# Kernel tuning notes

Measured on AMD Instinct MI355X. Metric: run time of the kernel, lower is better.

Reference implementation:

```python
import jax, jax.numpy as jnp
import numpy as np

N, C, T, V, K = 32, 256, 64, 25, 3   # batch, in_channels, frames, joints, adjacency partitions
D = 256                               # out_channels
KT = 9                                # temporal kernel size
PAD = (KT - 1) // 2
EPS = 1e-5                            # BatchNorm eps (torch default)


def setup_inputs() -> dict:
    key = jax.random.key(0)
    ks = jax.random.split(key, 5)
    x = jax.random.normal(ks[0], (N, C, T, V), jnp.float32)
    A = jax.random.uniform(ks[1], (K, V, V), jnp.float32)           # learnable adjacency
    W_gcn = jax.random.normal(ks[2], (K, D, C), jnp.float32) * (2.0 / C) ** 0.5  # K stacked 1x1 convs
    b_gcn = jnp.zeros((K, D), jnp.float32)
    W_tcn = jax.random.normal(ks[3], (D, D, KT, 1), jnp.float32) * (2.0 / (D * KT)) ** 0.5  # kaiming fan_out
    b_tcn = jnp.zeros((D,), jnp.float32)
    gamma = jnp.ones((D,), jnp.float32)   # bn_init(bn, 1)
    beta = jnp.zeros((D,), jnp.float32)
    return dict(x=x, A=A, W_gcn=W_gcn, b_gcn=b_gcn, W_tcn=W_tcn,
                b_tcn=b_tcn, gamma=gamma, beta=beta)


def reference(x, A, W_gcn, b_gcn, W_tcn, b_tcn, gamma, beta):
    # ---- GCN: per-partition 1x1 conv over channels, then graph aggregation via A[k], summed over k ----
    # y[k,n,d,t,v] = sum_c W_gcn[k,d,c] * x[n,c,t,v] + b_gcn[k,d]
    y = jnp.einsum('kdc,nctv->kndtv', W_gcn, x) + b_gcn[:, None, :, None, None]
    # aggregate neighbors: sum_v y[k,n,d,t,v] * A[k,v,w], accumulated over partitions k
    y = jnp.einsum('kndtv,kvw->ndtw', y, A)        # [N, D, T, V]

    # ---- TCN: (9,1) temporal conv + BatchNorm2d (batch statistics) ----
    z = jax.lax.conv_general_dilated(
        y, W_tcn, window_strides=(1, 1), padding=((PAD, PAD), (0, 0)),
        dimension_numbers=('NCHW', 'OIHW', 'NCHW'))
    z = z + b_tcn[None, :, None, None]
    mean = jnp.mean(z, axis=(0, 2, 3), keepdims=True)
    var = jnp.mean((z - mean) ** 2, axis=(0, 2, 3), keepdims=True)  # biased, as torch BN training fwd
    z = gamma[None, :, None, None] * (z - mean) * jax.lax.rsqrt(var + EPS) + beta[None, :, None, None]

    # ---- residual (identity branch: in==out, stride==1) + ReLU ----
    return jax.nn.relu(z + x)
```

## Files before the change

kernel.cpp:

```cpp
#include <hip/hip_runtime.h>
#include <math.h>

typedef unsigned short u16;
typedef short v8s __attribute__((ext_vector_type(8)));
typedef float v4f __attribute__((ext_vector_type(4)));

#define AS1 __attribute__((address_space(1)))
#define AS3 __attribute__((address_space(3)))

__device__ __forceinline__ float bf2f(u16 u) {
    union { unsigned int i; float f; } c; c.i = ((unsigned int)u) << 16; return c.f;
}
__device__ __forceinline__ u16 f2bf(float f) {
    union { float f; unsigned int i; } c; c.f = f;
    unsigned int u = c.i;
    return (u16)((u + 0x7FFFu + ((u >> 16) & 1u)) >> 16);
}
__device__ __forceinline__ void gload_lds16(const void* g, void* l) {
    __builtin_amdgcn_global_load_lds((const AS1 void*)(uintptr_t)g,
                                     (AS3 void*)(unsigned int)(uintptr_t)l,
                                     16, 0, 0);
}

#define Nn 32
#define Tt 64
#define Vv 25
#define NP 51200
#define NBLK 400

__global__ __launch_bounds__(256) void prep_kernel(
    const float* __restrict__ Wg, const float* __restrict__ Wt,
    const float* __restrict__ A, const float* __restrict__ bg,
    u16* __restrict__ Wgb, u16* __restrict__ Wtb,
    float* __restrict__ bias2, float* __restrict__ zpad)
{
    const int idx = blockIdx.x * 256 + threadIdx.x;
    const int stride = gridDim.x * 256;
    for (int i = idx; i < 256 * 2304; i += stride) {
        int d = i / 2304, r = i - d * 2304, dt = r >> 8, c = r & 255;
        Wtb[i] = f2bf(Wt[(d * 256 + c) * 9 + dt]);
    }
    for (int i = idx; i < 256 * 768; i += stride) {
        int d = i / 768, r = i - d * 768, k = r >> 8, c = r & 255;
        Wgb[i] = f2bf(Wg[(k * 256 + d) * 256 + c]);
    }
    for (int i = idx; i < 25 * 256; i += stride) {
        int w = i >> 8, d = i & 255;
        float s = 0.f;
        for (int k = 0; k < 3; ++k) {
            float cs = 0.f;
            for (int v = 0; v < 25; ++v) cs += A[(k * 25 + v) * 25 + w];
            s += bg[k * 256 + d] * cs;
        }
        bias2[i] = s;
    }
    for (int i = idx; i < 256; i += stride) zpad[i] = 0.f;
}

__global__ __launch_bounds__(256) void xa_kernel(
    const float* __restrict__ x, const float* __restrict__ A,
    u16* __restrict__ xa2)
{
    const int t = blockIdx.x, n = blockIdx.y;
    const int tid = threadIdx.x;
    __shared__ float xs[256 * 25];

    for (int i = tid; i < 6400; i += 256) {
        int c = i / 25, v = i - c * 25;
        xs[i] = x[((n * 256 + c) * 64 + t) * 25 + v];
    }
    __syncthreads();

    float xr[25];
    #pragma unroll
    for (int v = 0; v < 25; ++v) xr[v] = xs[tid * 25 + v];

    const size_t pbase = ((size_t)n * 64 + t) * 25;
    #pragma unroll 1
    for (int k = 0; k < 3; ++k) {
        float o[25];
        #pragma unroll
        for (int w = 0; w < 25; ++w) {
            float acc = 0.f;
            #pragma unroll
            for (int v = 0; v < 25; ++v)
                acc = fmaf(xr[v], A[(k * 25 + v) * 25 + w], acc);
            o[w] = acc;
        }
        u16* dst = xa2 + k * 256 + tid;
        #pragma unroll
        for (int w = 0; w < 25; ++w)
            dst[(pbase + w) * 768] = f2bf(o[w]);
    }
}

template<int KTOT, bool TCN>
__global__ __launch_bounds__(512, 2) void gemm_kernel(
    const u16* __restrict__ Ad, const u16* __restrict__ Bw,
    const float* __restrict__ bias, u16* __restrict__ outB,
    float* __restrict__ psum, float* __restrict__ psq,
    const u16* __restrict__ zpad)
{
    __shared__ u16 smem[24576];
    u16* As = smem;
    u16* Bs = smem + 8192;

    const int tid = threadIdx.x;
    const int wid = tid >> 6, lane = tid & 63;
    const int lr = lane & 15, hk = lane >> 4;
    const int wm = wid >> 2, wn = wid & 3;
    const int blk = blockIdx.x;
    const int rA = lane >> 3, sA = lane & 7;

    v4f acc[4][4];
    const v4f vzero = {0.f, 0.f, 0.f, 0.f};
    #pragma unroll
    for (int mf = 0; mf < 4; ++mf)
        #pragma unroll
        for (int nf = 0; nf < 4; ++nf) acc[mf][nf] = vzero;

    for (int kt = 0; kt < KTOT / 64; ++kt) {
        #pragma unroll
        for (int i = 0; i < 2; ++i) {
            const int ch = wid + i * 8;
            const int row = ch * 8 + rA;
            const int p = blk * 128 + row;
            const int ss = sA ^ (row & 7);
            const u16* src;
            if (TCN) {
                const int dt = kt >> 2, c0 = (kt & 3) << 6;
                const int tv = p % 1600, t = tv / 25;
                const int tp = t + dt - 4;
                const int p2 = p + (dt - 4) * 25;
                src = ((unsigned)tp < 64u) ? (Ad + (size_t)p2 * 256 + c0 + ss * 8) : zpad;
            } else {
                src = Ad + (size_t)p * 768 + kt * 64 + ss * 8;
            }
            gload_lds16(src, (char*)As + ch * 1024);
        }
        #pragma unroll
        for (int i = 0; i < 4; ++i) {
            const int ch = wid + i * 8;
            const int d = ch * 8 + rA;
            const int ss = sA ^ (d & 7);
            gload_lds16(Bw + (size_t)d * KTOT + kt * 64 + ss * 8, (char*)Bs + ch * 1024);
        }
        __syncthreads();

        v8s a[4][2], b[4][2];
        #pragma unroll
        for (int mf = 0; mf < 4; ++mf)
            #pragma unroll
            for (int kk = 0; kk < 2; ++kk) {
                const int row = wm * 64 + mf * 16 + lr;
                const int slot = kk * 4 + hk;
                a[mf][kk] = *(const v8s*)((const char*)As + row * 128 + ((slot ^ (row & 7)) << 4));
            }
        #pragma unroll
        for (int nf = 0; nf < 4; ++nf)
            #pragma unroll
            for (int kk = 0; kk < 2; ++kk) {
                const int row = wn * 64 + nf * 16 + lr;
                const int slot = kk * 4 + hk;
                b[nf][kk] = *(const v8s*)((const char*)Bs + row * 128 + ((slot ^ (row & 7)) << 4));
            }
        #pragma unroll
        for (int kk = 0; kk < 2; ++kk)
            #pragma unroll
            for (int mf = 0; mf < 4; ++mf)
                #pragma unroll
                for (int nf = 0; nf < 4; ++nf)
                    acc[mf][nf] = __builtin_amdgcn_mfma_f32_16x16x32_bf16(
                        a[mf][kk], b[nf][kk], acc[mf][nf], 0, 0, 0);
        __syncthreads();
    }

    if (!TCN) {
        #pragma unroll
        for (int mf = 0; mf < 4; ++mf) {
            #pragma unroll
            for (int j = 0; j < 4; ++j) {
                const int p = blk * 128 + wm * 64 + mf * 16 + hk * 4 + j;
                const int w = p % 25;
                #pragma unroll
                for (int nf = 0; nf < 4; ++nf) {
                    const int d = wn * 64 + nf * 16 + lr;
                    outB[(size_t)p * 256 + d] = f2bf(acc[mf][nf][j] + bias[w * 256 + d]);
                }
            }
        }
    } else {
        float s[4], q[4];
        #pragma unroll
        for (int nf = 0; nf < 4; ++nf) {
            const int d = wn * 64 + nf * 16 + lr;
            const float bb = bias[d];
            s[nf] = 0.f; q[nf] = 0.f;
            #pragma unroll
            for (int mf = 0; mf < 4; ++mf) {
                #pragma unroll
                for (int j = 0; j < 4; ++j) {
                    const int p = blk * 128 + wm * 64 + mf * 16 + hk * 4 + j;
                    const float zz = acc[mf][nf][j] + bb;
                    outB[(size_t)p * 256 + d] = f2bf(zz);
                    s[nf] += zz; q[nf] += zz * zz;
                }
            }
            s[nf] += __shfl_xor(s[nf], 16); s[nf] += __shfl_xor(s[nf], 32);
            q[nf] += __shfl_xor(q[nf], 16); q[nf] += __shfl_xor(q[nf], 32);
        }
        __syncthreads();
        float* red = (float*)smem;
        if (hk == 0) {
            #pragma unroll
            for (int nf = 0; nf < 4; ++nf) {
                const int d = wn * 64 + nf * 16 + lr;
                red[wm * 256 + d] = s[nf];
                red[512 + wm * 256 + d] = q[nf];
            }
        }
        __syncthreads();
        if (tid < 256) {
            psum[(size_t)tid * NBLK + blk] = red[tid] + red[256 + tid];
            psq[(size_t)tid * NBLK + blk]  = red[512 + tid] + red[768 + tid];
        }
    }
}

__global__ __launch_bounds__(256) void bn_stats_kernel(
    const float* __restrict__ psum, const float* __restrict__ psq,
    const float* __restrict__ gamma, const float* __restrict__ beta,
    float* __restrict__ scale, float* __restrict__ shift)
{
    const int d = blockIdx.x, tid = threadIdx.x;
    float s = 0.f, q = 0.f;
    for (int i = tid; i < NBLK; i += 256) {
        s += psum[(size_t)d * NBLK + i];
        q += psq[(size_t)d * NBLK + i];
    }
    #pragma unroll
    for (int off = 32; off; off >>= 1) {
        s += __shfl_down(s, off);
        q += __shfl_down(q, off);
    }
    __shared__ float rs[4], rq[4];
    if ((tid & 63) == 0) { rs[tid >> 6] = s; rq[tid >> 6] = q; }
    __syncthreads();
    if (tid == 0) {
        s = rs[0] + rs[1] + rs[2] + rs[3];
        q = rq[0] + rq[1] + rq[2] + rq[3];
        const float mean = s / 51200.f;
        const float var = q / 51200.f - mean * mean;
        const float inv = rsqrtf(var + 1e-5f);
        scale[d] = gamma[d] * inv;
        shift[d] = beta[d] - gamma[d] * inv * mean;
    }
}

__global__ __launch_bounds__(256) void bn_apply_kernel(
    const u16* __restrict__ zb, const float* __restrict__ x,
    const float* __restrict__ scale, const float* __restrict__ shift,
    float* __restrict__ out)
{
    const int chunk = blockIdx.x;
    const int n = blockIdx.y;
    const int tid = threadIdx.x;
    __shared__ u16 zs[128 * 66];
    const size_t p0 = (size_t)n * 1600 + chunk * 64;

    for (int half = 0; half < 2; ++half) {
        const int d0 = half * 128;
        if (half) __syncthreads();
        for (int i = tid; i < 128 * 64; i += 256) {
            const int pl = i >> 7, dl = i & 127;
            zs[dl * 66 + pl] = zb[(p0 + pl) * 256 + d0 + dl];
        }
        __syncthreads();
        for (int i = tid; i < 128 * 64; i += 256) {
            const int dl = i >> 6, j = i & 63;
            const int d = d0 + dl;
            const size_t addr = ((size_t)n * 256 + d) * 1600 + chunk * 64 + j;
            const float r = bf2f(zs[dl * 66 + j]) * scale[d] + shift[d] + x[addr];
            out[addr] = fmaxf(r, 0.f);
        }
    }
}

extern "C" void kernel_launch(void* const* d_in, const int* in_sizes, int n_in,
                              void* d_out, int out_size, void* d_ws, size_t ws_size,
                              hipStream_t stream)
{
    const float* x     = (const float*)d_in[0];
    const float* A     = (const float*)d_in[1];
    const float* Wg    = (const float*)d_in[2];
    const float* bg    = (const float*)d_in[3];
    const float* Wt    = (const float*)d_in[4];
    const float* bt    = (const float*)d_in[5];
    const float* gamma = (const float*)d_in[6];
    const float* beta  = (const float*)d_in[7];
    float* out = (float*)d_out;

    char* w = (char*)d_ws;
    u16*   xa2   = (u16*)(w);
    u16*   y2T   = (u16*)(w + 78643200);
    u16*   zb    = (u16*)(w + 104857600);
    u16*   Wgb   = (u16*)(w + 131072000);
    u16*   Wtb   = (u16*)(w + 131465216);
    float* bias2 = (float*)(w + 132644864);
    float* psum  = (float*)(w + 132670464);
    float* psq   = (float*)(w + 133080064);
    float* scale = (float*)(w + 133489664);
    float* shift = (float*)(w + 133490688);
    float* zpad  = (float*)(w + 133491712);

    prep_kernel<<<512, 256, 0, stream>>>(Wg, Wt, A, bg, Wgb, Wtb, bias2, zpad);
    xa_kernel<<<dim3(64, 32), 256, 0, stream>>>(x, A, xa2);
    gemm_kernel<768, false><<<NBLK, 512, 0, stream>>>(xa2, Wgb, bias2, y2T,
                                                      nullptr, nullptr, (const u16*)zpad);
    gemm_kernel<2304, true><<<NBLK, 512, 0, stream>>>(y2T, Wtb, bt, zb,
                                                      psum, psq, (const u16*)zpad);
    bn_stats_kernel<<<256, 256, 0, stream>>>(psum, psq, gamma, beta, scale, shift);
    bn_apply_kernel<<<dim3(25, 32), 256, 0, stream>>>(zb, x, scale, shift, out);
}
```

Measured before the change: 169.8 us.

## Enlarge GEMM tiles to 256x256 with XCD-aware block remapping

Both GEMM kernels now use 256-row by 256-column output tiles per block instead of 128x256, so each warp computes 8x4 MFMA fragments and the grid halves to 200 blocks. Block indices are remapped so consecutive M tiles land on the same XCD, and the prep kernel launches fewer blocks. This raises arithmetic intensity per LDS load and cuts redundant weight traffic, at the cost of more accumulator registers (occupancy hint dropped) and 200 blocks on 256 CUs leaving some CUs idle.

```diff
diff --git a/kernel.cpp b/kernel.cpp
--- a/kernel.cpp
+++ b/kernel.cpp
@@ -26,7 +26,7 @@
 #define Tt 64
 #define Vv 25
 #define NP 51200
-#define NBLK 400
+#define NBLK 200
 
 __global__ __launch_bounds__(256) void prep_kernel(
     const float* __restrict__ Wg, const float* __restrict__ Wt,
@@ -95,92 +95,89 @@
 }
 
 template<int KTOT, bool TCN>
-__global__ __launch_bounds__(512, 2) void gemm_kernel(
+__global__ __launch_bounds__(512) void gemm_kernel(
     const u16* __restrict__ Ad, const u16* __restrict__ Bw,
     const float* __restrict__ bias, u16* __restrict__ outB,
     float* __restrict__ psum, float* __restrict__ psq,
     const u16* __restrict__ zpad)
 {
-    __shared__ u16 smem[24576];
-    u16* As = smem;
-    u16* Bs = smem + 8192;
+    constexpr int NT = KTOT / 64;
+    __shared__ u16 smem[32768];
 
     const int tid = threadIdx.x;
     const int wid = tid >> 6, lane = tid & 63;
     const int lr = lane & 15, hk = lane >> 4;
     const int wm = wid >> 2, wn = wid & 3;
-    const int blk = blockIdx.x;
     const int rA = lane >> 3, sA = lane & 7;
 
-    v4f acc[4][4];
+    const int orig = blockIdx.x;
+    const int m = (orig & 7) * 25 + (orig >> 3);
+
+    u16* As = smem;
+    u16* Bs = smem + 16384;
+
+    v4f acc[8][4];
     const v4f vzero = {0.f, 0.f, 0.f, 0.f};
     #pragma unroll
-    for (int mf = 0; mf < 4; ++mf)
+    for (int mf = 0; mf < 8; ++mf)
         #pragma unroll
         for (int nf = 0; nf < 4; ++nf) acc[mf][nf] = vzero;
 
-    for (int kt = 0; kt < KTOT / 64; ++kt) {
-        #pragma unroll
-        for (int i = 0; i < 2; ++i) {
+    for (int kt = 0; kt < NT; ++kt) {
+        #pragma unroll
+        for (int i = 0; i < 4; ++i) {
             const int ch = wid + i * 8;
             const int row = ch * 8 + rA;
-            const int p = blk * 128 + row;
-            const int ss = sA ^ (row & 7);
-            const u16* src;
+            const int ss = sA ^ rA;
+            const u16* srcA;
             if (TCN) {
                 const int dt = kt >> 2, c0 = (kt & 3) << 6;
-                const int tv = p % 1600, t = tv / 25;
+                const int p = m * 256 + row;
+                const int t = (p % 1600) / 25;
                 const int tp = t + dt - 4;
-                const int p2 = p + (dt - 4) * 25;
-                src = ((unsigned)tp < 64u) ? (Ad + (size_t)p2 * 256 + c0 + ss * 8) : zpad;
+                srcA = ((unsigned)tp < 64u)
+                     ? (Ad + (size_t)(p + (dt - 4) * 25) * 256 + c0 + ss * 8)
+                     : zpad;
             } else {
-                src = Ad + (size_t)p * 768 + kt * 64 + ss * 8;
-            }
-            gload_lds16(src, (char*)As + ch * 1024);
-        }
-        #pragma unroll
-        for (int i = 0; i < 4; ++i) {
-            const int ch = wid + i * 8;
-            const int d = ch * 8 + rA;
-            const int ss = sA ^ (d & 7);
-            gload_lds16(Bw + (size_t)d * KTOT + kt * 64 + ss * 8, (char*)Bs + ch * 1024);
-        }
-        __syncthreads();
-
-        v8s a[4][2], b[4][2];
-        #pragma unroll
-        for (int mf = 0; mf < 4; ++mf)
-            #pragma unroll
-            for (int kk = 0; kk < 2; ++kk) {
-                const int row = wm * 64 + mf * 16 + lr;
+                srcA = Ad + (size_t)(m * 256 + row) * 768 + kt * 64 + ss * 8;
+            }
+            gload_lds16(srcA, (char*)As + ch * 1024);
+            gload_lds16(Bw + (size_t)row * KTOT + kt * 64 + ss * 8,
+                        (char*)Bs + ch * 1024);
+        }
+        __syncthreads();
+
+        #pragma unroll
+        for (int kk = 0; kk < 2; ++kk) {
+            v8s a[8], b[4];
+            #pragma unroll
+            for (int mf = 0; mf < 8; ++mf) {
+                const int row = wm * 128 + mf * 16 + lr;
                 const int slot = kk * 4 + hk;
-                a[mf][kk] = *(const v8s*)((const char*)As + row * 128 + ((slot ^ (row & 7)) << 4));
-            }
-        #pragma unroll
-        for (int nf = 0; nf < 4; ++nf)
-            #pragma unroll
-            for (int kk = 0; kk < 2; ++kk) {
+                a[mf] = *(const v8s*)((const char*)As + row * 128 + ((slot ^ (row & 7)) << 4));
+            }
+            #pragma unroll
+            for (int nf = 0; nf < 4; ++nf) {
                 const int row = wn * 64 + nf * 16 + lr;
                 const int slot = kk * 4 + hk;
-                b[nf][kk] = *(const v8s*)((const char*)Bs + row * 128 + ((slot ^ (row & 7)) << 4));
-            }
-        #pragma unroll
-        for (int kk = 0; kk < 2; ++kk)
-            #pragma unroll
-            for (int mf = 0; mf < 4; ++mf)
+                b[nf] = *(const v8s*)((const char*)Bs + row * 128 + ((slot ^ (row & 7)) << 4));
+            }
+            #pragma unroll
+            for (int mf = 0; mf < 8; ++mf)
                 #pragma unroll
                 for (int nf = 0; nf < 4; ++nf)
                     acc[mf][nf] = __builtin_amdgcn_mfma_f32_16x16x32_bf16(
-                        a[mf][kk], b[nf][kk], acc[mf][nf], 0, 0, 0);
+                        a[mf], b[nf], acc[mf][nf], 0, 0, 0);
+        }
         __syncthreads();
     }
 
     if (!TCN) {
         #pragma unroll
-        for (int mf = 0; mf < 4; ++mf) {
+        for (int mf = 0; mf < 8; ++mf) {
             #pragma unroll
             for (int j = 0; j < 4; ++j) {
-                const int p = blk * 128 + wm * 64 + mf * 16 + hk * 4 + j;
+                const int p = m * 256 + wm * 128 + mf * 16 + hk * 4 + j;
                 const int w = p % 25;
                 #pragma unroll
                 for (int nf = 0; nf < 4; ++nf) {
@@ -197,10 +194,10 @@
             const float bb = bias[d];
             s[nf] = 0.f; q[nf] = 0.f;
             #pragma unroll
-            for (int mf = 0; mf < 4; ++mf) {
+            for (int mf = 0; mf < 8; ++mf) {
                 #pragma unroll
                 for (int j = 0; j < 4; ++j) {
-                    const int p = blk * 128 + wm * 64 + mf * 16 + hk * 4 + j;
+                    const int p = m * 256 + wm * 128 + mf * 16 + hk * 4 + j;
                     const float zz = acc[mf][nf][j] + bb;
                     outB[(size_t)p * 256 + d] = f2bf(zz);
                     s[nf] += zz; q[nf] += zz * zz;
@@ -221,8 +218,8 @@
         }
         __syncthreads();
         if (tid < 256) {
-            psum[(size_t)tid * NBLK + blk] = red[tid] + red[256 + tid];
-            psq[(size_t)tid * NBLK + blk]  = red[512 + tid] + red[768 + tid];
+            psum[(size_t)tid * NBLK + m] = red[tid] + red[256 + tid];
+            psq[(size_t)tid * NBLK + m]  = red[512 + tid] + red[768 + tid];
         }
     }
 }
@@ -313,7 +310,7 @@
     float* shift = (float*)(w + 133490688);
     float* zpad  = (float*)(w + 133491712);
 
-    prep_kernel<<<512, 256, 0, stream>>>(Wg, Wt, A, bg, Wgb, Wtb, bias2, zpad);
+    prep_kernel<<<128, 256, 0, stream>>>(Wg, Wt, A, bg, Wgb, Wtb, bias2, zpad);
     xa_kernel<<<dim3(64, 32), 256, 0, stream>>>(x, A, xa2);
     gemm_kernel<768, false><<<NBLK, 512, 0, stream>>>(xa2, Wgb, bias2, y2T,
                                                       nullptr, nullptr, (const u16*)zpad);
```

Measured after the change: 196.8 us. +15.9%, slower.

## Restructure temporal conv GEMM to reuse a haloed LDS tile across taps

Applied to the files above, without the earlier changes.

The temporal convolution kernel now loads one 128-row activation tile plus a 104-row halo on each side into LDS once per 64-channel chunk. All 9 temporal taps are computed from that single tile by shifting the row index, instead of reloading an im2col slice for every tap. Weights are pre-permuted into MFMA fragment order and read straight from global memory into registers with double buffering, so B no longer goes through LDS. Boundary blocks zero the out-of-range tap fragments, and both GEMMs use a block index remap. The cost is a larger LDS footprint per block, extra work to load the halo, and a masked code path for blocks near sequence edges.

```diff
diff --git a/kernel.cpp b/kernel.cpp
--- a/kernel.cpp
+++ b/kernel.cpp
@@ -31,18 +31,22 @@
 __global__ __launch_bounds__(256) void prep_kernel(
     const float* __restrict__ Wg, const float* __restrict__ Wt,
     const float* __restrict__ A, const float* __restrict__ bg,
-    u16* __restrict__ Wgb, u16* __restrict__ Wtb,
+    u16* __restrict__ Wgb, u16* __restrict__ Bpt,
     float* __restrict__ bias2, float* __restrict__ zpad)
 {
     const int idx = blockIdx.x * 256 + threadIdx.x;
     const int stride = gridDim.x * 256;
-    for (int i = idx; i < 256 * 2304; i += stride) {
-        int d = i / 2304, r = i - d * 2304, dt = r >> 8, c = r & 255;
-        Wtb[i] = f2bf(Wt[(d * 256 + c) * 9 + dt]);
+    for (int i = idx; i < 589824; i += stride) {
+        const int e = i & 7, lane = (i >> 3) & 63, sub = i >> 9;
+        const int kk = sub & 1, nf = (sub >> 1) & 3, wn = (sub >> 3) & 3;
+        const int cc = (sub >> 5) & 3, dt = sub >> 7;
+        const int d = wn * 64 + nf * 16 + (lane & 15);
+        const int c = cc * 64 + kk * 32 + (lane >> 4) * 8 + e;
+        Bpt[i] = f2bf(Wt[(d * 256 + c) * 9 + dt]);
     }
     for (int i = idx; i < 256 * 768; i += stride) {
-        int d = i / 768, r = i - d * 768, k = r >> 8, c = r & 255;
-        Wgb[i] = f2bf(Wg[(k * 256 + d) * 256 + c]);
+        int d = i / 768, r = i - d * 768, k3 = r >> 8, c = r & 255;
+        Wgb[i] = f2bf(Wg[(k3 * 256 + d) * 256 + c]);
     }
     for (int i = idx; i < 25 * 256; i += stride) {
         int w = i >> 8, d = i & 255;
@@ -94,12 +98,9 @@
     }
 }
 
-template<int KTOT, bool TCN>
-__global__ __launch_bounds__(512, 2) void gemm_kernel(
+__global__ __launch_bounds__(512) void gemm1_kernel(
     const u16* __restrict__ Ad, const u16* __restrict__ Bw,
-    const float* __restrict__ bias, u16* __restrict__ outB,
-    float* __restrict__ psum, float* __restrict__ psq,
-    const u16* __restrict__ zpad)
+    const float* __restrict__ bias, u16* __restrict__ outB)
 {
     __shared__ u16 smem[24576];
     u16* As = smem;
@@ -109,8 +110,10 @@
     const int wid = tid >> 6, lane = tid & 63;
     const int lr = lane & 15, hk = lane >> 4;
     const int wm = wid >> 2, wn = wid & 3;
-    const int blk = blockIdx.x;
     const int rA = lane >> 3, sA = lane & 7;
+
+    const int orig = blockIdx.x;
+    const int m = (orig & 7) * 50 + (orig >> 3);
 
     v4f acc[4][4];
     const v4f vzero = {0.f, 0.f, 0.f, 0.f};
@@ -119,31 +122,22 @@
         #pragma unroll
         for (int nf = 0; nf < 4; ++nf) acc[mf][nf] = vzero;
 
-    for (int kt = 0; kt < KTOT / 64; ++kt) {
+    for (int kt = 0; kt < 12; ++kt) {
         #pragma unroll
         for (int i = 0; i < 2; ++i) {
             const int ch = wid + i * 8;
             const int row = ch * 8 + rA;
-            const int p = blk * 128 + row;
-            const int ss = sA ^ (row & 7);
-            const u16* src;
-            if (TCN) {
-                const int dt = kt >> 2, c0 = (kt & 3) << 6;
-                const int tv = p % 1600, t = tv / 25;
-                const int tp = t + dt - 4;
-                const int p2 = p + (dt - 4) * 25;
-                src = ((unsigned)tp < 64u) ? (Ad + (size_t)p2 * 256 + c0 + ss * 8) : zpad;
-            } else {
-                src = Ad + (size_t)p * 768 + kt * 64 + ss * 8;
-            }
-            gload_lds16(src, (char*)As + ch * 1024);
+            const int ss = sA ^ rA;
+            gload_lds16(Ad + (size_t)(m * 128 + row) * 768 + kt * 64 + ss * 8,
+                        (char*)As + ch * 1024);
         }
         #pragma unroll
         for (int i = 0; i < 4; ++i) {
             const int ch = wid + i * 8;
             const int d = ch * 8 + rA;
-            const int ss = sA ^ (d & 7);
-            gload_lds16(Bw + (size_t)d * KTOT + kt * 64 + ss * 8, (char*)Bs + ch * 1024);
+            const int ss = sA ^ rA;
+            gload_lds16(Bw + (size_t)d * 768 + kt * 64 + ss * 8,
+                        (char*)Bs + ch * 1024);
         }
         __syncthreads();
 
@@ -175,55 +169,149 @@
         __syncthreads();
     }
 
-    if (!TCN) {
+    #pragma unroll
+    for (int mf = 0; mf < 4; ++mf) {
+        #pragma unroll
+        for (int j = 0; j < 4; ++j) {
+            const int p = m * 128 + wm * 64 + mf * 16 + hk * 4 + j;
+            const int w = p % 25;
+            #pragma unroll
+            for (int nf = 0; nf < 4; ++nf) {
+                const int d = wn * 64 + nf * 16 + lr;
+                outB[(size_t)p * 256 + d] = f2bf(acc[mf][nf][j] + bias[w * 256 + d]);
+            }
+        }
+    }
+}
+
+__global__ __launch_bounds__(512) void tcn_halo_kernel(
+    const u16* __restrict__ y2T, const u16* __restrict__ Bpt,
+    const float* __restrict__ bt, u16* __restrict__ zb,
+    float* __restrict__ psum, float* __restrict__ psq,
+    const u16* __restrict__ zp)
+{
+    __shared__ u16 smem[21504];
+
+    const int tid = threadIdx.x;
+    const int wid = tid >> 6, lane = tid & 63;
+    const int lr = lane & 15, hk = lane >> 4;
+    const int wm = wid >> 2, wn = wid & 3;
+    const int rA = lane >> 3, sA = lane & 7;
+
+    const int orig = blockIdx.x;
+    const int m = (orig & 7) * 50 + (orig >> 3);
+
+    u16* As = smem;
+
+    v4f acc[4][4];
+    const v4f vzero = {0.f, 0.f, 0.f, 0.f};
+    #pragma unroll
+    for (int mf = 0; mf < 4; ++mf)
+        #pragma unroll
+        for (int nf = 0; nf < 4; ++nf) acc[mf][nf] = vzero;
+
+    int tt[4];
+    #pragma unroll
+    for (int mf = 0; mf < 4; ++mf)
+        tt[mf] = ((m * 128 + wm * 64 + mf * 16 + lr) % 1600) / 25;
+
+    const int r0 = (m * 128) % 1600;
+    const bool safe = (r0 >= 104) && (r0 <= 1368);
+
+#define BLOAD(bank, dtv, ccv)                                                  \
+    {                                                                          \
+        const u16* bw = Bpt + ((((dtv)*4 + (ccv)) * 4 + wn) << 12) + lane * 8; \
+        _Pragma("unroll")                                                      \
+        for (int nf = 0; nf < 4; ++nf)                                         \
+            _Pragma("unroll")                                                  \
+            for (int kk = 0; kk < 2; ++kk)                                     \
+                bb[bank][nf][kk] = *(const v8s*)(bw + ((nf * 2 + kk) << 9));   \
+    }
+
+#define CC_BODY(MASKED)                                                        \
+    _Pragma("unroll 1")                                                        \
+    for (int cc = 0; cc < 4; ++cc) {                                           \
+        if (cc) __syncthreads();                                               \
+        for (int ch = wid; ch < 42; ch += 8) {                                 \
+            const int row = ch * 8 + rA;                                       \
+            const int srow = m * 128 - 104 + row;                              \
+            const int ss = sA ^ rA;                                            \
+            const u16* src = ((unsigned)srow < 51200u)                         \
+                ? (y2T + (size_t)srow * 256 + cc * 64 + ss * 8) : zp;          \
+            gload_lds16(src, (char*)As + ch * 1024);                           \
+        }                                                                      \
+        __syncthreads();                                                       \
+        v8s bb[2][4][2];                                                       \
+        BLOAD(0, 0, cc)                                                        \
+        _Pragma("unroll")                                                      \
+        for (int dt = 0; dt < 9; ++dt) {                                       \
+            if (dt < 8) BLOAD((dt + 1) & 1, dt + 1, cc)                        \
+            v8s a[4][2];                                                       \
+            _Pragma("unroll")                                                  \
+            for (int mf = 0; mf < 4; ++mf)                                     \
+                _Pragma("unroll")                                              \
+                for (int kk = 0; kk < 2; ++kk) {                               \
+                    const int lrow = 104 + wm * 64 + mf * 16 + lr + (dt - 4) * 25; \
+                    const int slot = kk * 4 + hk;                              \
+                    a[mf][kk] = *(const v8s*)((const char*)As + lrow * 128 +   \
+                                              ((slot ^ (lrow & 7)) << 4));     \
+                }                                                              \
+            if (MASKED) {                                                      \
+                _Pragma("unroll")                                              \
+                for (int mf = 0; mf < 4; ++mf) {                               \
+                    const bool ok = (unsigned)(tt[mf] + dt - 4) < 64u;         \
+                    a[mf][0] = ok ? a[mf][0] : (v8s)(short)0;                  \
+                    a[mf][1] = ok ? a[mf][1] : (v8s)(short)0;                  \
+                }                                                              \
+            }                                                                  \
+            _Pragma("unroll")                                                  \
+            for (int kk = 0; kk < 2; ++kk)                                     \
+                _Pragma("unroll")                                              \
+                for (int mf = 0; mf < 4; ++mf)                                 \
+                    _Pragma("unroll")                                          \
+                    for (int nf = 0; nf < 4; ++nf)                             \
+                        acc[mf][nf] = __builtin_amdgcn_mfma_f32_16x16x32_bf16( \
+                            a[mf][kk], bb[dt & 1][nf][kk], acc[mf][nf], 0, 0, 0); \
+        }                                                                      \
+    }
+
+    if (safe) { CC_BODY(false) } else { CC_BODY(true) }
+#undef CC_BODY
+#undef BLOAD
+
+    float s[4], q[4];
+    #pragma unroll
+    for (int nf = 0; nf < 4; ++nf) {
+        const int d = wn * 64 + nf * 16 + lr;
+        const float bbv = bt[d];
+        s[nf] = 0.f; q[nf] = 0.f;
         #pragma unroll
         for (int mf = 0; mf < 4; ++mf) {
             #pragma unroll
             for (int j = 0; j < 4; ++j) {
-                const int p = blk * 128 + wm * 64 + mf * 16 + hk * 4 + j;
-                const int w = p % 25;
-                #pragma unroll
-                for (int nf = 0; nf < 4; ++nf) {
-                    const int d = wn * 64 + nf * 16 + lr;
-                    outB[(size_t)p * 256 + d] = f2bf(acc[mf][nf][j] + bias[w * 256 + d]);
-                }
+                const int p = m * 128 + wm * 64 + mf * 16 + hk * 4 + j;
+                const float zz = acc[mf][nf][j] + bbv;
+                zb[(size_t)p * 256 + d] = f2bf(zz);
+                s[nf] += zz; q[nf] += zz * zz;
             }
         }
-    } else {
-        float s[4], q[4];
+        s[nf] += __shfl_xor(s[nf], 16); s[nf] += __shfl_xor(s[nf], 32);
+        q[nf] += __shfl_xor(q[nf], 16); q[nf] += __shfl_xor(q[nf], 32);
+    }
+    __syncthreads();
+    float* red = (float*)smem;
+    if (hk == 0) {
         #pragma unroll
         for (int nf = 0; nf < 4; ++nf) {
             const int d = wn * 64 + nf * 16 + lr;
-            const float bb = bias[d];
-            s[nf] = 0.f; q[nf] = 0.f;
-            #pragma unroll
-            for (int mf = 0; mf < 4; ++mf) {
-                #pragma unroll
-                for (int j = 0; j < 4; ++j) {
-                    const int p = blk * 128 + wm * 64 + mf * 16 + hk * 4 + j;
-                    const float zz = acc[mf][nf][j] + bb;
-                    outB[(size_t)p * 256 + d] = f2bf(zz);
-                    s[nf] += zz; q[nf] += zz * zz;
-                }
-            }
-            s[nf] += __shfl_xor(s[nf], 16); s[nf] += __shfl_xor(s[nf], 32);
-            q[nf] += __shfl_xor(q[nf], 16); q[nf] += __shfl_xor(q[nf], 32);
-        }
-        __syncthreads();
-        float* red = (float*)smem;
-        if (hk == 0) {
-            #pragma unroll
-            for (int nf = 0; nf < 4; ++nf) {
-                const int d = wn * 64 + nf * 16 + lr;
-                red[wm * 256 + d] = s[nf];
-                red[512 + wm * 256 + d] = q[nf];
-            }
-        }
-        __syncthreads();
-        if (tid < 256) {
-            psum[(size_t)tid * NBLK + blk] = red[tid] + red[256 + tid];
-            psq[(size_t)tid * NBLK + blk]  = red[512 + tid] + red[768 + tid];
-        }
+            red[wm * 256 + d] = s[nf];
+            red[512 + wm * 256 + d] = q[nf];
+        }
+    }
+    __syncthreads();
+    if (tid < 256) {
+        psum[(size_t)tid * NBLK + m] = red[tid] + red[256 + tid];
+        psq[(size_t)tid * NBLK + m]  = red[512 + tid] + red[768 + tid];
     }
 }
 
@@ -305,7 +393,7 @@
     u16*   y2T   = (u16*)(w + 78643200);
     u16*   zb    = (u16*)(w + 104857600);
     u16*   Wgb   = (u16*)(w + 131072000);
-    u16*   Wtb   = (u16*)(w + 131465216);
+    u16*   Bpt   = (u16*)(w + 131465216);
     float* bias2 = (float*)(w + 132644864);
     float* psum  = (float*)(w + 132670464);
     float* psq   = (float*)(w + 133080064);
@@ -313,12 +401,11 @@
     float* shift = (float*)(w + 133490688);
     float* zpad  = (float*)(w + 133491712);
 
-    prep_kernel<<<512, 256, 0, stream>>>(Wg, Wt, A, bg, Wgb, Wtb, bias2, zpad);
+    prep_kernel<<<256, 256, 0, stream>>>(Wg, Wt, A, bg, Wgb, Bpt, bias2, zpad);
     xa_kernel<<<dim3(64, 32), 256, 0, stream>>>(x, A, xa2);
-    gemm_kernel<768, false><<<NBLK, 512, 0, stream>>>(xa2, Wgb, bias2, y2T,
-                                                      nullptr, nullptr, (const u16*)zpad);
-    gemm_kernel<2304, true><<<NBLK, 512, 0, stream>>>(y2T, Wtb, bt, zb,
-                                                      psum, psq, (const u16*)zpad);
+    gemm1_kernel<<<NBLK, 512, 0, stream>>>(xa2, Wgb, bias2, y2T);
+    tcn_halo_kernel<<<NBLK, 512, 0, stream>>>(y2T, Bpt, bt, zb, psum, psq,
+                                              (const u16*)zpad);
     bn_stats_kernel<<<256, 256, 0, stream>>>(psum, psq, gamma, beta, scale, shift);
     bn_apply_kernel<<<dim3(25, 32), 256, 0, stream>>>(zb, x, scale, shift, out);
 }
```

New measurement: 172.7 us. No clear change (+1.7%).

## Split TCN GEMM K dimension in two and move BN stats to separate pass

Applied to the files above, without the earlier changes.

Splits the temporal-conv GEMM over its reduction dimension into two halves run as 800 blocks, each writing a bf16 partial result, so the 400-block grid fills more of the GPU. BN statistics move out of the GEMM epilogue into a new zsum kernel that adds the two partials, and bn_apply now sums both partials itself. It also adds an XCD-aware block index swizzle, drops the min-occupancy launch bound, and halves the prep grid. In exchange it adds extra memory traffic for the second partial buffer and an extra kernel launch, and it rounds each partial to bf16 before summing.

```diff
diff --git a/kernel.cpp b/kernel.cpp
--- a/kernel.cpp
+++ b/kernel.cpp
@@ -94,12 +94,9 @@
     }
 }
 
-template<int KTOT, bool TCN>
-__global__ __launch_bounds__(512, 2) void gemm_kernel(
+__global__ __launch_bounds__(512) void gemm1_kernel(
     const u16* __restrict__ Ad, const u16* __restrict__ Bw,
-    const float* __restrict__ bias, u16* __restrict__ outB,
-    float* __restrict__ psum, float* __restrict__ psq,
-    const u16* __restrict__ zpad)
+    const float* __restrict__ bias, u16* __restrict__ outB)
 {
     __shared__ u16 smem[24576];
     u16* As = smem;
@@ -109,8 +106,10 @@
     const int wid = tid >> 6, lane = tid & 63;
     const int lr = lane & 15, hk = lane >> 4;
     const int wm = wid >> 2, wn = wid & 3;
-    const int blk = blockIdx.x;
     const int rA = lane >> 3, sA = lane & 7;
+
+    const int orig = blockIdx.x;
+    const int m = (orig & 7) * 50 + (orig >> 3);
 
     v4f acc[4][4];
     const v4f vzero = {0.f, 0.f, 0.f, 0.f};
@@ -119,31 +118,22 @@
         #pragma unroll
         for (int nf = 0; nf < 4; ++nf) acc[mf][nf] = vzero;
 
-    for (int kt = 0; kt < KTOT / 64; ++kt) {
+    for (int kt = 0; kt < 12; ++kt) {
         #pragma unroll
         for (int i = 0; i < 2; ++i) {
             const int ch = wid + i * 8;
             const int row = ch * 8 + rA;
-            const int p = blk * 128 + row;
-            const int ss = sA ^ (row & 7);
-            const u16* src;
-            if (TCN) {
-                const int dt = kt >> 2, c0 = (kt & 3) << 6;
-                const int tv = p % 1600, t = tv / 25;
-                const int tp = t + dt - 4;
-                const int p2 = p + (dt - 4) * 25;
-                src = ((unsigned)tp < 64u) ? (Ad + (size_t)p2 * 256 + c0 + ss * 8) : zpad;
-            } else {
-                src = Ad + (size_t)p * 768 + kt * 64 + ss * 8;
-            }
-            gload_lds16(src, (char*)As + ch * 1024);
+            const int ss = sA ^ rA;
+            gload_lds16(Ad + (size_t)(m * 128 + row) * 768 + kt * 64 + ss * 8,
+                        (char*)As + ch * 1024);
         }
         #pragma unroll
         for (int i = 0; i < 4; ++i) {
             const int ch = wid + i * 8;
             const int d = ch * 8 + rA;
-            const int ss = sA ^ (d & 7);
-            gload_lds16(Bw + (size_t)d * KTOT + kt * 64 + ss * 8, (char*)Bs + ch * 1024);
+            const int ss = sA ^ rA;
+            gload_lds16(Bw + (size_t)d * 768 + kt * 64 + ss * 8,
+                        (char*)Bs + ch * 1024);
         }
         __syncthreads();
 
@@ -175,56 +165,133 @@
         __syncthreads();
     }
 
-    if (!TCN) {
-        #pragma unroll
-        for (int mf = 0; mf < 4; ++mf) {
-            #pragma unroll
-            for (int j = 0; j < 4; ++j) {
-                const int p = blk * 128 + wm * 64 + mf * 16 + hk * 4 + j;
-                const int w = p % 25;
-                #pragma unroll
-                for (int nf = 0; nf < 4; ++nf) {
-                    const int d = wn * 64 + nf * 16 + lr;
-                    outB[(size_t)p * 256 + d] = f2bf(acc[mf][nf][j] + bias[w * 256 + d]);
-                }
-            }
-        }
-    } else {
-        float s[4], q[4];
-        #pragma unroll
-        for (int nf = 0; nf < 4; ++nf) {
-            const int d = wn * 64 + nf * 16 + lr;
-            const float bb = bias[d];
-            s[nf] = 0.f; q[nf] = 0.f;
-            #pragma unroll
-            for (int mf = 0; mf < 4; ++mf) {
-                #pragma unroll
-                for (int j = 0; j < 4; ++j) {
-                    const int p = blk * 128 + wm * 64 + mf * 16 + hk * 4 + j;
-                    const float zz = acc[mf][nf][j] + bb;
-                    outB[(size_t)p * 256 + d] = f2bf(zz);
-                    s[nf] += zz; q[nf] += zz * zz;
-                }
-            }
-            s[nf] += __shfl_xor(s[nf], 16); s[nf] += __shfl_xor(s[nf], 32);
-            q[nf] += __shfl_xor(q[nf], 16); q[nf] += __shfl_xor(q[nf], 32);
-        }
-        __syncthreads();
-        float* red = (float*)smem;
-        if (hk == 0) {
+    #pragma unroll
+    for (int mf = 0; mf < 4; ++mf) {
+        #pragma unroll
+        for (int j = 0; j < 4; ++j) {
+            const int p = m * 128 + wm * 64 + mf * 16 + hk * 4 + j;
+            const int w = p % 25;
             #pragma unroll
             for (int nf = 0; nf < 4; ++nf) {
                 const int d = wn * 64 + nf * 16 + lr;
-                red[wm * 256 + d] = s[nf];
-                red[512 + wm * 256 + d] = q[nf];
-            }
-        }
-        __syncthreads();
-        if (tid < 256) {
-            psum[(size_t)tid * NBLK + blk] = red[tid] + red[256 + tid];
-            psq[(size_t)tid * NBLK + blk]  = red[512 + tid] + red[768 + tid];
-        }
-    }
+                outB[(size_t)p * 256 + d] = f2bf(acc[mf][nf][j] + bias[w * 256 + d]);
+            }
+        }
+    }
+}
+
+__global__ __launch_bounds__(512) void tcn_split_kernel(
+    const u16* __restrict__ y2T, const u16* __restrict__ Wtb,
+    const float* __restrict__ bt, u16* __restrict__ zb1,
+    u16* __restrict__ zb2, const u16* __restrict__ zpad)
+{
+    __shared__ u16 smem[24576];
+    u16* As = smem;
+    u16* Bs = smem + 8192;
+
+    const int tid = threadIdx.x;
+    const int wid = tid >> 6, lane = tid & 63;
+    const int lr = lane & 15, hk = lane >> 4;
+    const int wm = wid >> 2, wn = wid & 3;
+    const int rA = lane >> 3, sA = lane & 7;
+
+    const int orig = blockIdx.x;
+    const int swz = (orig & 7) * 100 + (orig >> 3);
+    const int split = swz / 400, m = swz % 400;
+    const int kt0 = split * 18;
+    u16* zbo = split ? zb2 : zb1;
+
+    v4f acc[4][4];
+    const v4f vzero = {0.f, 0.f, 0.f, 0.f};
+    #pragma unroll
+    for (int mf = 0; mf < 4; ++mf)
+        #pragma unroll
+        for (int nf = 0; nf < 4; ++nf) acc[mf][nf] = vzero;
+
+    for (int kt = kt0; kt < kt0 + 18; ++kt) {
+        #pragma unroll
+        for (int i = 0; i < 2; ++i) {
+            const int ch = wid + i * 8;
+            const int row = ch * 8 + rA;
+            const int ss = sA ^ rA;
+            const int dt = kt >> 2, c0 = (kt & 3) << 6;
+            const int p = m * 128 + row;
+            const int t = (p % 1600) / 25;
+            const int tp = t + dt - 4;
+            const u16* srcA = ((unsigned)tp < 64u)
+                 ? (y2T + (size_t)(p + (dt - 4) * 25) * 256 + c0 + ss * 8)
+                 : zpad;
+            gload_lds16(srcA, (char*)As + ch * 1024);
+        }
+        #pragma unroll
+        for (int i = 0; i < 4; ++i) {
+            const int ch = wid + i * 8;
+            const int d = ch * 8 + rA;
+            const int ss = sA ^ rA;
+            gload_lds16(Wtb + (size_t)d * 2304 + kt * 64 + ss * 8,
+                        (char*)Bs + ch * 1024);
+        }
+        __syncthreads();
+
+        v8s a[4][2], b[4][2];
+        #pragma unroll
+        for (int mf = 0; mf < 4; ++mf)
+            #pragma unroll
+            for (int kk = 0; kk < 2; ++kk) {
+                const int row = wm * 64 + mf * 16 + lr;
+                const int slot = kk * 4 + hk;
+                a[mf][kk] = *(const v8s*)((const char*)As + row * 128 + ((slot ^ (row & 7)) << 4));
+            }
+        #pragma unroll
+        for (int nf = 0; nf < 4; ++nf)
+            #pragma unroll
+            for (int kk = 0; kk < 2; ++kk) {
+                const int row = wn * 64 + nf * 16 + lr;
+                const int slot = kk * 4 + hk;
+                b[nf][kk] = *(const v8s*)((const char*)Bs + row * 128 + ((slot ^ (row & 7)) << 4));
+            }
+        #pragma unroll
+        for (int kk = 0; kk < 2; ++kk)
+            #pragma unroll
+            for (int mf = 0; mf < 4; ++mf)
+                #pragma unroll
+                for (int nf = 0; nf < 4; ++nf)
+                    acc[mf][nf] = __builtin_amdgcn_mfma_f32_16x16x32_bf16(
+                        a[mf][kk], b[nf][kk], acc[mf][nf], 0, 0, 0);
+        __syncthreads();
+    }
+
+    #pragma unroll
+    for (int nf = 0; nf < 4; ++nf) {
+        const int d = wn * 64 + nf * 16 + lr;
+        const float bb = split ? 0.f : bt[d];
+        #pragma unroll
+        for (int mf = 0; mf < 4; ++mf) {
+            #pragma unroll
+            for (int j = 0; j < 4; ++j) {
+                const int p = m * 128 + wm * 64 + mf * 16 + hk * 4 + j;
+                zbo[(size_t)p * 256 + d] = f2bf(acc[mf][nf][j] + bb);
+            }
+        }
+    }
+}
+
+__global__ __launch_bounds__(256) void zsum_kernel(
+    const u16* __restrict__ zb1, const u16* __restrict__ zb2,
+    float* __restrict__ psum, float* __restrict__ psq)
+{
+    const int m = blockIdx.x;
+    const int d = threadIdx.x;
+    const u16* r1 = zb1 + (size_t)m * 128 * 256 + d;
+    const u16* r2 = zb2 + (size_t)m * 128 * 256 + d;
+    float s = 0.f, q = 0.f;
+    #pragma unroll 4
+    for (int r = 0; r < 128; ++r) {
+        const float z = bf2f(r1[r * 256]) + bf2f(r2[r * 256]);
+        s += z; q += z * z;
+    }
+    psum[(size_t)d * NBLK + m] = s;
+    psq[(size_t)d * NBLK + m]  = q;
 }
 
 __global__ __launch_bounds__(256) void bn_stats_kernel(
@@ -258,14 +325,14 @@
 }
 
 __global__ __launch_bounds__(256) void bn_apply_kernel(
-    const u16* __restrict__ zb, const float* __restrict__ x,
-    const float* __restrict__ scale, const float* __restrict__ shift,
-    float* __restrict__ out)
+    const u16* __restrict__ zb1, const u16* __restrict__ zb2,
+    const float* __restrict__ x, const float* __restrict__ scale,
+    const float* __restrict__ shift, float* __restrict__ out)
 {
     const int chunk = blockIdx.x;
     const int n = blockIdx.y;
     const int tid = threadIdx.x;
-    __shared__ u16 zs[128 * 66];
+    __shared__ float zs[128 * 66];
     const size_t p0 = (size_t)n * 1600 + chunk * 64;
 
     for (int half = 0; half < 2; ++half) {
@@ -273,14 +340,15 @@
         if (half) __syncthreads();
         for (int i = tid; i < 128 * 64; i += 256) {
             const int pl = i >> 7, dl = i & 127;
-            zs[dl * 66 + pl] = zb[(p0 + pl) * 256 + d0 + dl];
+            const size_t idx = (p0 + pl) * 256 + d0 + dl;
+            zs[dl * 66 + pl] = bf2f(zb1[idx]) + bf2f(zb2[idx]);
         }
         __syncthreads();
         for (int i = tid; i < 128 * 64; i += 256) {
             const int dl = i >> 6, j = i & 63;
             const int d = d0 + dl;
             const size_t addr = ((size_t)n * 256 + d) * 1600 + chunk * 64 + j;
-            const float r = bf2f(zs[dl * 66 + j]) * scale[d] + shift[d] + x[addr];
+            const float r = zs[dl * 66 + j] * scale[d] + shift[d] + x[addr];
             out[addr] = fmaxf(r, 0.f);
         }
     }
@@ -302,8 +370,9 @@
 
     char* w = (char*)d_ws;
     u16*   xa2   = (u16*)(w);
+    u16*   zb1   = (u16*)(w);
     u16*   y2T   = (u16*)(w + 78643200);
-    u16*   zb    = (u16*)(w + 104857600);
+    u16*   zb2   = (u16*)(w + 104857600);
     u16*   Wgb   = (u16*)(w + 131072000);
     u16*   Wtb   = (u16*)(w + 131465216);
     float* bias2 = (float*)(w + 132644864);
@@ -313,12 +382,12 @@
     float* shift = (float*)(w + 133490688);
     float* zpad  = (float*)(w + 133491712);
 
-    prep_kernel<<<512, 256, 0, stream>>>(Wg, Wt, A, bg, Wgb, Wtb, bias2, zpad);
+    prep_kernel<<<256, 256, 0, stream>>>(Wg, Wt, A, bg, Wgb, Wtb, bias2, zpad);
     xa_kernel<<<dim3(64, 32), 256, 0, stream>>>(x, A, xa2);
-    gemm_kernel<768, false><<<NBLK, 512, 0, stream>>>(xa2, Wgb, bias2, y2T,
-                                                      nullptr, nullptr, (const u16*)zpad);
-    gemm_kernel<2304, true><<<NBLK, 512, 0, stream>>>(y2T, Wtb, bt, zb,
-                                                      psum, psq, (const u16*)zpad);
+    gemm1_kernel<<<NBLK, 512, 0, stream>>>(xa2, Wgb, bias2, y2T);
+    tcn_split_kernel<<<800, 512, 0, stream>>>(y2T, Wtb, bt, zb1, zb2,
+                                              (const u16*)zpad);
+    zsum_kernel<<<NBLK, 256, 0, stream>>>(zb1, zb2, psum, psq);
     bn_stats_kernel<<<256, 256, 0, stream>>>(psum, psq, gamma, beta, scale, shift);
-    bn_apply_kernel<<<dim3(25, 32), 256, 0, stream>>>(zb, x, scale, shift, out);
-}
+    bn_apply_kernel<<<dim3(25, 32), 256, 0, stream>>>(zb1, zb2, x, scale, shift, out);
+}
```

New measurement: 200.7 us. 1.18x slower.
